# Kernel optimization log

Hardware: AMD Instinct MI355X
Metric: run time of the kernel (lower is better)

Reference implementation:

```python
import jax, jax.numpy as jnp
import numpy as np
import math

EPS = 1e-8
H, DM, S = 16, 1024, 128  # heads, d_model, seq_len (== channels)
DK = DM // H


def _fq_act_uint8(x):
    # Brevitas Uint8ActPerTensorFloat: per-tensor unsigned 8-bit fake-quant (negatives clip to 0)
    s = jnp.maximum(jnp.max(x), EPS) / 255.0
    return jnp.clip(jnp.round(x / s), 0.0, 255.0) * s


def _fq_w_int8(w):
    # Int8 weight per-tensor, narrow range [-127, 127]
    s = jnp.maximum(jnp.max(jnp.abs(w)), EPS) / 127.0
    return jnp.clip(jnp.round(w / s), -127.0, 127.0) * s, s


def _fq_pc_int8(x, axis):
    # QuantIdentity: signed 8-bit fake-quant, per-channel scale along `axis` (abs-max stats)
    red = tuple(i for i in range(x.ndim) if i != axis)
    s = jnp.maximum(jnp.max(jnp.abs(x), axis=red, keepdims=True), EPS) / 127.0
    return jnp.clip(jnp.round(x / s), -128.0, 127.0) * s


def _quant_linear(x, W, b):
    # QuantLinear: uint8 input quant, int8 weight quant, Int32 bias quant (scale = s_in * s_w)
    s_in = jnp.maximum(jnp.max(x), EPS) / 255.0
    xq = jnp.clip(jnp.round(x / s_in), 0.0, 255.0) * s_in
    Wq, s_w = _fq_w_int8(W)
    s_b = s_in * s_w
    bq = jnp.round(b / s_b) * s_b
    return jnp.einsum('bsd,od->bso', xq, Wq) + bq


def setup_inputs() -> dict:
    key = jax.random.key(0)
    ks = jax.random.split(key, 12)
    B = 64
    std = 1.0 / math.sqrt(DM)
    inp = {
        'query': jax.random.normal(ks[0], (B, S, DM), jnp.float32),
        'key':   jax.random.normal(ks[1], (B, S, DM), jnp.float32),
        'value': jax.random.normal(ks[2], (B, S, DM), jnp.float32),
        'mask':  jnp.ones((B, S, S), jnp.int32),
    }
    for i, nm in enumerate(['q', 'k', 'v', 'o']):
        inp[f'W{nm}'] = jax.random.normal(ks[3 + i], (DM, DM), jnp.float32) * std
        inp[f'b{nm}'] = jax.random.normal(ks[7 + i], (DM,), jnp.float32) * 0.01
    return inp


def reference(query, key, value, mask, Wq, bq, Wk, bk, Wv, bv, Wo, bo):
    B = query.shape[0]
    # QuantLinear projections -> [B, h, S, d_k]
    def proj(x, W, b):
        return _quant_linear(x, W, b).reshape(B, S, H, DK).transpose(0, 2, 1, 3)
    q = proj(query, Wq, bq)
    k = proj(key, Wk, bk)
    v = proj(value, Wv, bv)

    # quantizer_1: per-channel on q rows (axis 2); quantizer_2: on k^T columns (axis 3)
    kt = jnp.swapaxes(k, -2, -1)  # [B, h, d_k, S]
    scores = jnp.matmul(_fq_pc_int8(q, 2), _fq_pc_int8(kt, 3)) / math.sqrt(DK)
    scores = jnp.where(mask[:, None, :, :] == 0, -1e9, scores)
    p_attn = jax.nn.softmax(scores, axis=-1)

    # quantizer_3: per-channel on p_attn columns (axis 3); quantizer_4: on v rows (axis 2)
    x = jnp.matmul(_fq_pc_int8(p_attn, 3), _fq_pc_int8(v, 2))  # [B, h, S, d_k]
    x = x.transpose(0, 2, 1, 3).reshape(B, S, DM)
    return _quant_linear(x, Wo, bo)
```

## Files before the change

kernel.cpp:

```cpp
#include <hip/hip_runtime.h>
#include <hip/hip_bf16.h>
#include <math.h>

typedef unsigned short u16;
typedef unsigned int u32;
typedef unsigned long long u64;
typedef signed char i8;

constexpr int NB = 64, NS = 128, NDM = 1024, NH = 16, NDK = 64;
constexpr int NM = NB * NS;
constexpr float QEPS = 1e-8f;

typedef __attribute__((ext_vector_type(8))) short short8;
typedef __attribute__((ext_vector_type(4))) float f32x4;
typedef __attribute__((ext_vector_type(4))) int i32x4;

__device__ __forceinline__ u32 fenc(float f) {
  u32 u = __float_as_uint(f);
  return (u & 0x80000000u) ? ~u : (u | 0x80000000u);
}
__device__ __forceinline__ float fdec(u32 u) {
  u = (u & 0x80000000u) ? (u & 0x7FFFFFFFu) : ~u;
  return __uint_as_float(u);
}
__device__ __forceinline__ u16 f2bf(float f) { return (u16)(__float_as_uint(f) >> 16); }
__device__ __forceinline__ float bf2f(u16 u) { return __uint_as_float(((u32)u) << 16); }

__device__ __forceinline__ void glds16(const void* g, void* l) {
  __builtin_amdgcn_global_load_lds(
      (const __attribute__((address_space(1))) void*)(unsigned long long)(uintptr_t)g,
      (__attribute__((address_space(3))) void*)(u32)(uintptr_t)l, 16, 0, 0);
}


__global__ void maskbits_kernel(const int* __restrict__ mask, u64* __restrict__ mb,
                                u32* __restrict__ scl) {
  if (blockIdx.x == 0) {
    for (int i = threadIdx.x; i < 2048; i += blockDim.x) scl[i] = 0u;
  }
  int row = blockIdx.x * 4 + (threadIdx.x >> 6);
  int lane = threadIdx.x & 63;
  const int* mrow = mask + (size_t)row * NS;
  u64 b0 = __ballot(mrow[lane] != 0);
  u64 b1 = __ballot(mrow[64 + lane] != 0);
  if (lane == 0) { mb[row * 2] = b0; mb[row * 2 + 1] = b1; }
}

__global__ void fused_max_kernel(const float* __restrict__ q, const float* __restrict__ k,
                                 const float* __restrict__ v, const float* __restrict__ w0,
                                 const float* __restrict__ w1, const float* __restrict__ w2,
                                 const float* __restrict__ w3, u32* __restrict__ sclu) {
  int y = blockIdx.y;
  const float* src; size_t n4; int ab;
  switch (y) {
    case 0: src = q; n4 = (size_t)NM * NDM / 4; ab = 0; break;
    case 1: src = k; n4 = (size_t)NM * NDM / 4; ab = 0; break;
    case 2: src = v; n4 = (size_t)NM * NDM / 4; ab = 0; break;
    case 3: src = w0; n4 = (size_t)NDM * NDM / 4; ab = 1; break;
    case 4: src = w1; n4 = (size_t)NDM * NDM / 4; ab = 1; break;
    case 5: src = w2; n4 = (size_t)NDM * NDM / 4; ab = 1; break;
    default: src = w3; n4 = (size_t)NDM * NDM / 4; ab = 1; break;
  }
  float m = -INFINITY;
  size_t stride = (size_t)gridDim.x * blockDim.x;
  for (size_t i = (size_t)blockIdx.x * blockDim.x + threadIdx.x; i < n4; i += stride) {
    float4 f = ((const float4*)src)[i];
    if (ab) { f.x = fabsf(f.x); f.y = fabsf(f.y); f.z = fabsf(f.z); f.w = fabsf(f.w); }
    m = fmaxf(m, fmaxf(fmaxf(f.x, f.y), fmaxf(f.z, f.w)));
  }
  for (int off = 32; off; off >>= 1) m = fmaxf(m, __shfl_down(m, off));
  __shared__ float sm[4];
  if ((threadIdx.x & 63) == 0) sm[threadIdx.x >> 6] = m;
  __syncthreads();
  if (threadIdx.x == 0) {
    float r = fmaxf(fmaxf(sm[0], sm[1]), fmaxf(sm[2], sm[3]));
    atomicMax(&sclu[y], fenc(r));
  }
}

__global__ __launch_bounds__(256)
void quant_w_i8_kernel(const float* __restrict__ w0, const float* __restrict__ w1,
                       const float* __restrict__ w2, const float* __restrict__ w3,
                       i8* __restrict__ dst, int* __restrict__ colsum,
                       const u32* __restrict__ sclu) {
  int y = blockIdx.y, row = blockIdx.x, tid = threadIdx.x;
  const float* src = (y == 0 ? w0 : y == 1 ? w1 : y == 2 ? w2 : w3) + (size_t)row * NDM;
  float s = fmaxf(fdec(sclu[3 + y]), QEPS) / 127.0f;
  float4 f = ((const float4*)src)[tid];
  int a = (int)fminf(fmaxf(rintf(f.x / s), -127.f), 127.f);
  int b = (int)fminf(fmaxf(rintf(f.y / s), -127.f), 127.f);
  int c = (int)fminf(fmaxf(rintf(f.z / s), -127.f), 127.f);
  int d = (int)fminf(fmaxf(rintf(f.w / s), -127.f), 127.f);
  ((int*)(dst + (size_t)y * NDM * NDM + (size_t)row * NDM))[tid] =
      (a & 255) | ((b & 255) << 8) | ((c & 255) << 16) | ((d & 255) << 24);
  int ssum = a + b + c + d;
  for (int off = 32; off; off >>= 1) ssum += __shfl_down(ssum, off);
  __shared__ int sm[4];
  if ((tid & 63) == 0) sm[tid >> 6] = ssum;
  __syncthreads();
  if (tid == 0) colsum[y * NDM + row] = sm[0] + sm[1] + sm[2] + sm[3];
}

__global__ void quant_a_kernel(const float* __restrict__ s0, const float* __restrict__ s1,
                               const float* __restrict__ s2, i8* __restrict__ dst,
                               const u32* __restrict__ sclu, int slot_base) {
  int y = blockIdx.y;
  const float* src = y == 0 ? s0 : y == 1 ? s1 : s2;
  i8* d = dst + (size_t)y * NM * NDM;
  float s = fmaxf(fdec(sclu[slot_base + y]), QEPS) / 255.0f;
  size_t n4 = (size_t)NM * NDM / 4;
  size_t stride = (size_t)gridDim.x * blockDim.x;
  for (size_t i = (size_t)blockIdx.x * blockDim.x + threadIdx.x; i < n4; i += stride) {
    float4 f = ((const float4*)src)[i];
    int a = (int)fminf(fmaxf(rintf(f.x / s), 0.f), 255.f) - 128;
    int b = (int)fminf(fmaxf(rintf(f.y / s), 0.f), 255.f) - 128;
    int c = (int)fminf(fmaxf(rintf(f.z / s), 0.f), 255.f) - 128;
    int e = (int)fminf(fmaxf(rintf(f.w / s), 0.f), 255.f) - 128;
    ((int*)d)[i] = (a & 255) | ((b & 255) << 8) | ((c & 255) << 16) | ((e & 255) << 24);
  }
}

__global__ void qkv_i8_kernel(const float* __restrict__ projbase, i8* __restrict__ dstbase,
                              const float* __restrict__ scl) {
  int y = blockIdx.y;
  const float* src = projbase + (size_t)y * NM * NDM;
  i8* dst = dstbase + (size_t)y * NM * NDM;
  const float* sb = scl + 8 + y * 128;
  size_t n4 = (size_t)NM * NDM / 4;
  size_t stride = (size_t)gridDim.x * blockDim.x;
  for (size_t i = (size_t)blockIdx.x * blockDim.x + threadIdx.x; i < n4; i += stride) {
    int s_idx = (int)((i >> 8) & 127);
    float s = fmaxf(sb[s_idx], QEPS) / 127.0f;
    float4 f = ((const float4*)src)[i];
    int a = (int)fminf(fmaxf(rintf(f.x / s), -128.f), 127.f);
    int b = (int)fminf(fmaxf(rintf(f.y / s), -128.f), 127.f);
    int c = (int)fminf(fmaxf(rintf(f.z / s), -128.f), 127.f);
    int d = (int)fminf(fmaxf(rintf(f.w / s), -128.f), 127.f);
    ((int*)dst)[i] = (a & 255) | ((b & 255) << 8) | ((c & 255) << 16) | ((d & 255) << 24);
  }
}

constexpr int BM = 128, BN = 128, BK = 64;

template <bool PROJ>
__global__ __launch_bounds__(256)
void gemm_kernel(const i8* __restrict__ Abase, const i8* __restrict__ Wbase,
                 const int* __restrict__ colsum, const float* __restrict__ b0,
                 const float* __restrict__ b1, const float* __restrict__ b2,
                 float* __restrict__ Cbase, u32* __restrict__ sclu) {
  constexpr int K = NDM, N = NDM;
  const int z = PROJ ? blockIdx.z : 0;
  const i8* A = Abase + (size_t)z * NM * NDM;
  const i8* Wt = PROJ ? (Wbase + (size_t)z * NDM * NDM) : Wbase;
  const float* bias = PROJ ? (z == 0 ? b0 : z == 1 ? b1 : b2) : b0;
  float* C = PROJ ? (Cbase + (size_t)z * NM * NDM) : Cbase;
  const u32* slot_in = PROJ ? (sclu + z) : (sclu + 7);
  const u32* slot_w = PROJ ? (sclu + 3 + z) : (sclu + 6);
  const int* cs = colsum + (PROJ ? z : 3) * NDM;

  __shared__ __align__(16) i8 As[BM][BK];
  __shared__ __align__(16) i8 Bs[BN][BK];
  __shared__ float rmax2[2][BM];

  const int tid = threadIdx.x;
  const int lane = tid & 63, wave = tid >> 6;
  const int wm = (wave & 1) * 64, wn = (wave >> 1) * 64;
  const int r16 = lane & 15, quad = lane >> 4;
  const int bm = blockIdx.x * BM, bn = blockIdx.y * BN;

  i32x4 acc[4][4] = {};

  const int lrow = lane >> 2, lcol = (lane & 3) * 16;
  for (int k0 = 0; k0 < K; k0 += BK) {
    __syncthreads();
#pragma unroll
    for (int p = 0; p < 2; p++) {
      int r = wave * 32 + p * 16;
      glds16(A + (size_t)(bm + r + lrow) * K + k0 + lcol, &As[r][0]);
      glds16(Wt + (size_t)(bn + r + lrow) * K + k0 + lcol, &Bs[r][0]);
    }
    __syncthreads();
    i32x4 af[4], bfr[4];
#pragma unroll
    for (int i = 0; i < 4; i++) af[i] = *(const i32x4*)(&As[wm + i * 16 + r16][quad * 16]);
#pragma unroll
    for (int j = 0; j < 4; j++) bfr[j] = *(const i32x4*)(&Bs[wn + j * 16 + r16][quad * 16]);
#pragma unroll
    for (int i = 0; i < 4; i++)
#pragma unroll
      for (int j = 0; j < 4; j++)
        acc[i][j] = __builtin_amdgcn_mfma_i32_16x16x64_i8(af[i], bfr[j], acc[i][j], 0, 0, 0);
  }

  float s_in = fmaxf(fdec(*slot_in), QEPS) / 255.0f;
  float s_w = fmaxf(fdec(*slot_w), QEPS) / 127.0f;
  float sc = s_in * s_w;

  float bq[4];
  int csj[4];
#pragma unroll
  for (int j = 0; j < 4; j++) {
    int gc = bn + wn + j * 16 + r16;
    bq[j] = rintf(bias[gc] / sc) * sc;
    csj[j] = cs[gc] << 7;
  }
#pragma unroll
  for (int i = 0; i < 4; i++) {
#pragma unroll
    for (int r = 0; r < 4; r++) {
      int lr = wm + i * 16 + quad * 4 + r;
      int gr = bm + lr;
      float rm = 0.0f;
#pragma unroll
      for (int j = 0; j < 4; j++) {
        int gc = bn + wn + j * 16 + r16;
        float val = (float)(acc[i][j][r] + csj[j]) * sc + bq[j];
        C[(size_t)gr * N + gc] = val;
        if (PROJ) rm = fmaxf(rm, fabsf(val));
      }
      if (PROJ) {
#pragma unroll
        for (int off = 1; off < 16; off <<= 1) rm = fmaxf(rm, __shfl_xor(rm, off));
        if (r16 == 0) rmax2[wave >> 1][lr] = rm;
      }
    }
  }
  if (PROJ) {
    __syncthreads();
    if (tid < BM) {
      float m = fmaxf(rmax2[0][tid], rmax2[1][tid]);
      atomicMax((int*)&sclu[8 + z * 128 + tid], __float_as_int(m));
    }
  }
}

__global__ __launch_bounds__(256)
void attn_colmax_kernel(const i8* __restrict__ qi8, const i8* __restrict__ ki8,
                        const u64* __restrict__ mb, const float* __restrict__ scl,
                        float* __restrict__ cm_part) {
  const int bh = blockIdx.x, b = bh >> 4, h = bh & 15;
  const int tid = threadIdx.x, lane = tid & 63, wave = tid >> 6;
  const int r16 = lane & 15, quad = lane >> 4;

  __shared__ __align__(16) i8 Qs[NS][80];
  __shared__ __align__(16) i8 Ks[NS][80];
  __shared__ float sqv[NS], skv[NS];
  __shared__ float cmw[4][NS];

  {
    int row = tid >> 1, half = (tid & 1) * 32;
    const i8* qp = qi8 + (size_t)(b * NS + row) * NDM + h * NDK + half;
    const i8* kp = ki8 + (size_t)(b * NS + row) * NDM + h * NDK + half;
    *(int4*)&Qs[row][half] = *(const int4*)qp;
    *(int4*)&Qs[row][half + 16] = *(const int4*)(qp + 16);
    *(int4*)&Ks[row][half] = *(const int4*)kp;
    *(int4*)&Ks[row][half + 16] = *(const int4*)(kp + 16);
    if (tid < NS) {
      sqv[tid] = fmaxf(scl[8 + tid], QEPS) / 127.0f;
      skv[tid] = fmaxf(scl[8 + 128 + tid], QEPS) / 127.0f;
    }
  }
  __syncthreads();

  const int rowbase = wave * 32;
  i32x4 acc[2][8] = {};
#pragma unroll
  for (int mt = 0; mt < 2; mt++) {
    i32x4 a = *(const i32x4*)&Qs[rowbase + mt * 16 + r16][quad * 16];
#pragma unroll
    for (int nt = 0; nt < 8; nt++) {
      i32x4 bfrag = *(const i32x4*)&Ks[nt * 16 + r16][quad * 16];
      acc[mt][nt] = __builtin_amdgcn_mfma_i32_16x16x64_i8(a, bfrag, acc[mt][nt], 0, 0, 0);
    }
  }

  float skc[8], cm[8];
#pragma unroll
  for (int nt = 0; nt < 8; nt++) { skc[nt] = skv[nt * 16 + r16]; cm[nt] = 0.0f; }

#pragma unroll
  for (int mt = 0; mt < 2; mt++) {
#pragma unroll
    for (int r = 0; r < 4; r++) {
      int row = rowbase + mt * 16 + quad * 4 + r;
      float sq = sqv[row];
      const u64* mrow = mb + ((size_t)b * NS + row) * 2;
      u64 m0 = mrow[0], m1 = mrow[1];
      float vals[8];
      float mx = -INFINITY;
#pragma unroll
      for (int nt = 0; nt < 8; nt++) {
        float v = (float)acc[mt][nt][r] * (sq * skc[nt]) * 0.125f;
        u64 bits = nt < 4 ? m0 : m1;
        if (((bits >> ((nt * 16 + r16) & 63)) & 1ull) == 0) v = -1e9f;
        vals[nt] = v;
        mx = fmaxf(mx, v);
      }
#pragma unroll
      for (int off = 1; off < 16; off <<= 1) mx = fmaxf(mx, __shfl_xor(mx, off));
      float sum = 0.0f;
#pragma unroll
      for (int nt = 0; nt < 8; nt++) { vals[nt] = __expf(vals[nt] - mx); sum += vals[nt]; }
#pragma unroll
      for (int off = 1; off < 16; off <<= 1) sum += __shfl_xor(sum, off);
#pragma unroll
      for (int nt = 0; nt < 8; nt++) {
        float p = vals[nt] / sum;
        cm[nt] = fmaxf(cm[nt], p);
      }
    }
  }

#pragma unroll
  for (int nt = 0; nt < 8; nt++) {
    float c = cm[nt];
    c = fmaxf(c, __shfl_xor(c, 16));
    c = fmaxf(c, __shfl_xor(c, 32));
    if (quad == 0) cmw[wave][nt * 16 + r16] = c;
  }
  __syncthreads();
  if (tid < NS) {
    float c = fmaxf(fmaxf(cmw[0][tid], cmw[1][tid]), fmaxf(cmw[2][tid], cmw[3][tid]));
    cm_part[(size_t)tid * (NB * NH) + bh] = c;
  }
}

__global__ void colmax_reduce_kernel(const float* __restrict__ cm_part,
                                     u32* __restrict__ sclu) {
  int j = blockIdx.x;
  const float* row = cm_part + (size_t)j * (NB * NH);
  float m = 0.0f;
  for (int i = threadIdx.x; i < NB * NH; i += blockDim.x) m = fmaxf(m, row[i]);
  for (int off = 32; off; off >>= 1) m = fmaxf(m, __shfl_down(m, off));
  __shared__ float sm[4];
  if ((threadIdx.x & 63) == 0) sm[threadIdx.x >> 6] = m;
  __syncthreads();
  if (threadIdx.x == 0)
    sclu[392 + j] = __float_as_uint(fmaxf(fmaxf(sm[0], sm[1]), fmaxf(sm[2], sm[3])));
}

__global__ __launch_bounds__(256, 4)
void attn_pv2_kernel(const i8* __restrict__ qi8, const i8* __restrict__ ki8,
                     const i8* __restrict__ vi8, const u64* __restrict__ mb,
                     const float* __restrict__ scl, float* __restrict__ xout,
                     u32* __restrict__ xmax_slot) {
  const int bh = blockIdx.x, b = bh >> 4, h = bh & 15;
  const int tid = threadIdx.x, lane = tid & 63, wave = tid >> 6;
  const int r16 = lane & 15, quad = lane >> 4;
  const int rowbase = wave * 32;

  union SU {
    i8 K[NS][64];
    struct { u16 hi[64][72]; u16 lo[64][72]; } v;
  };
  __shared__ __align__(16) SU u;
  __shared__ __align__(16) u16 Ps[NS][72];
  __shared__ float sqv[NS], skv[NS], spv[NS], svv[NS];
  __shared__ float xmw[4];

  const int jl = tid >> 2, d0v = (tid & 3) * 16;
  const i8* vb = vi8 + (size_t)(b * NS + jl) * NDM + h * NDK + d0v;
  int4 vpre0 = *(const int4*)vb;
  int4 vpre1 = *(const int4*)(vb + (size_t)64 * NDM);

  i32x4 aq[2];
  {
    const i8* qp = qi8 + (size_t)b * NS * NDM + h * NDK;
#pragma unroll
    for (int mt = 0; mt < 2; mt++)
      aq[mt] = *(const i32x4*)(qp + (size_t)(rowbase + mt * 16 + r16) * NDM + quad * 16);
    const int lrow = lane >> 2, lcol = (lane & 3) * 16;
#pragma unroll
    for (int p = 0; p < 2; p++) {
      int r = wave * 32 + p * 16;
      glds16(ki8 + (size_t)(b * NS + r + lrow) * NDM + h * NDK + lcol, &u.K[r][0]);
    }
    if (tid < NS) {
      sqv[tid] = fmaxf(scl[8 + tid], QEPS) / 127.0f;
      skv[tid] = fmaxf(scl[8 + 128 + tid], QEPS) / 127.0f;
      spv[tid] = fmaxf(scl[392 + tid], QEPS) / 127.0f;
      svv[tid] = fmaxf(scl[8 + 256 + tid], QEPS) / 127.0f;
    }
  }
  __syncthreads();

  i32x4 acc[2][8] = {};
  __builtin_amdgcn_s_setprio(1);
#pragma unroll
  for (int mt = 0; mt < 2; mt++) {
#pragma unroll
    for (int nt = 0; nt < 8; nt++) {
      i32x4 bfrag = *(const i32x4*)&u.K[nt * 16 + r16][quad * 16];
      acc[mt][nt] = __builtin_amdgcn_mfma_i32_16x16x64_i8(aq[mt], bfrag, acc[mt][nt], 0, 0, 0);
    }
  }
  __builtin_amdgcn_s_setprio(0);

  float skc[8], spc[8];
#pragma unroll
  for (int nt = 0; nt < 8; nt++) {
    skc[nt] = skv[nt * 16 + r16];
    spc[nt] = spv[nt * 16 + r16];
  }

  u32 pqh[2][4][2];
#pragma unroll
  for (int mt = 0; mt < 2; mt++) {
#pragma unroll
    for (int r = 0; r < 4; r++) {
      int row = rowbase + mt * 16 + quad * 4 + r;
      float sq = sqv[row];
      const u64* mrow = mb + ((size_t)b * NS + row) * 2;
      u64 m0 = mrow[0], m1 = mrow[1];
      float vals[8];
      float mx = -INFINITY;
#pragma unroll
      for (int nt = 0; nt < 8; nt++) {
        float v = (float)acc[mt][nt][r] * (sq * skc[nt]) * 0.125f;
        u64 bits = nt < 4 ? m0 : m1;
        if (((bits >> ((nt * 16 + r16) & 63)) & 1ull) == 0) v = -1e9f;
        vals[nt] = v;
        mx = fmaxf(mx, v);
      }
#pragma unroll
      for (int off = 1; off < 16; off <<= 1) mx = fmaxf(mx, __shfl_xor(mx, off));
      float sum = 0.0f;
#pragma unroll
      for (int nt = 0; nt < 8; nt++) { vals[nt] = __expf(vals[nt] - mx); sum += vals[nt]; }
#pragma unroll
      for (int off = 1; off < 16; off <<= 1) sum += __shfl_xor(sum, off);
#pragma unroll
      for (int nt = 0; nt < 4; nt++) {
        float p = vals[nt] / sum;
        float pq = fminf(fmaxf(rintf(p / spc[nt]), -128.f), 127.f);
        Ps[row][nt * 16 + r16] = f2bf(pq);
      }
#pragma unroll
      for (int n2 = 0; n2 < 2; n2++) {
        float pa_ = vals[4 + n2 * 2] / sum;
        float pb_ = vals[5 + n2 * 2] / sum;
        float qa = fminf(fmaxf(rintf(pa_ / spc[4 + n2 * 2]), -128.f), 127.f);
        float qb = fminf(fmaxf(rintf(pb_ / spc[5 + n2 * 2]), -128.f), 127.f);
        pqh[mt][r][n2] = (u32)f2bf(qa) | ((u32)f2bf(qb) << 16);
      }
    }
  }

  f32x4 xacc[2][4] = {};
#pragma unroll
  for (int half = 0; half < 2; half++) {
    __syncthreads();
    {
      int j = half * 64 + jl;
      float g = spv[j] * svv[j];
      int4 raw = half ? vpre1 : vpre0;
      const i8* rb = (const i8*)&raw;
#pragma unroll
      for (int d = 0; d < 16; d++) {
        float w = (float)rb[d] * g;
        u16 hi = f2bf(w);
        u.v.hi[d0v + d][jl] = hi;
        u.v.lo[d0v + d][jl] = f2bf(w - bf2f(hi));
      }
    }
    __syncthreads();
    __builtin_amdgcn_s_setprio(1);
#pragma unroll
    for (int kk = 0; kk < 2; kk++) {
      short8 pa[2];
#pragma unroll
      for (int mt = 0; mt < 2; mt++)
        pa[mt] = *(const short8*)&Ps[rowbase + mt * 16 + r16][kk * 32 + quad * 8];
#pragma unroll
      for (int nt = 0; nt < 4; nt++) {
        short8 vh = *(const short8*)&u.v.hi[nt * 16 + r16][kk * 32 + quad * 8];
        short8 vl = *(const short8*)&u.v.lo[nt * 16 + r16][kk * 32 + quad * 8];
#pragma unroll
        for (int mt = 0; mt < 2; mt++) {
          xacc[mt][nt] = __builtin_amdgcn_mfma_f32_16x16x32_bf16(pa[mt], vh, xacc[mt][nt], 0, 0, 0);
          xacc[mt][nt] = __builtin_amdgcn_mfma_f32_16x16x32_bf16(pa[mt], vl, xacc[mt][nt], 0, 0, 0);
        }
      }
    }
    __builtin_amdgcn_s_setprio(0);
    if (half == 0) {
#pragma unroll
      for (int mt = 0; mt < 2; mt++)
#pragma unroll
        for (int r = 0; r < 4; r++) {
          int row = rowbase + mt * 16 + quad * 4 + r;
#pragma unroll
          for (int n2 = 0; n2 < 2; n2++) {
            u32 pk = pqh[mt][r][n2];
            Ps[row][(n2 * 2) * 16 + r16] = (u16)(pk & 0xFFFFu);
            Ps[row][(n2 * 2 + 1) * 16 + r16] = (u16)(pk >> 16);
          }
        }
    }
  }

  float mx = -INFINITY;
#pragma unroll
  for (int mt = 0; mt < 2; mt++)
#pragma unroll
    for (int nt = 0; nt < 4; nt++)
#pragma unroll
      for (int r = 0; r < 4; r++) {
        int row = rowbase + mt * 16 + quad * 4 + r;
        xout[((size_t)b * NS + row) * NDM + h * NDK + nt * 16 + r16] = xacc[mt][nt][r];
        mx = fmaxf(mx, xacc[mt][nt][r]);
      }
#pragma unroll
  for (int off = 1; off < 64; off <<= 1) mx = fmaxf(mx, __shfl_xor(mx, off));
  if (lane == 0) xmw[wave] = mx;
  __syncthreads();
  if (tid == 0) {
    float m = fmaxf(fmaxf(xmw[0], xmw[1]), fmaxf(xmw[2], xmw[3]));
    atomicMax(xmax_slot, fenc(m));
  }
}

constexpr size_t OFF_SCL = 0;
constexpr size_t OFF_CS  = 8192;
constexpr size_t OFF_MB  = OFF_CS + 4 * NDM * 4;
constexpr size_t OFF_W   = OFF_MB + (size_t)NM * 16;
constexpr size_t OFF_XQ  = OFF_W + 4 * (size_t)NDM * NDM;
constexpr size_t OFF_PQ  = OFF_XQ + 3 * (size_t)NM * NDM;
constexpr size_t OFF_I8  = OFF_PQ + 3 * (size_t)NM * NDM * 4;
constexpr size_t OFF_CM  = OFF_I8 + 3 * (size_t)NM * NDM;

extern "C" void kernel_launch(void* const* d_in, const int* in_sizes, int n_in,
                              void* d_out, int out_size, void* d_ws, size_t ws_size,
                              hipStream_t stream) {
  const float* query = (const float*)d_in[0];
  const float* key = (const float*)d_in[1];
  const float* value = (const float*)d_in[2];
  const int* mask = (const int*)d_in[3];
  const float* Wq = (const float*)d_in[4]; const float* bq = (const float*)d_in[5];
  const float* Wk = (const float*)d_in[6]; const float* bk = (const float*)d_in[7];
  const float* Wv = (const float*)d_in[8]; const float* bv = (const float*)d_in[9];
  const float* Wo = (const float*)d_in[10]; const float* bo = (const float*)d_in[11];

  char* ws = (char*)d_ws;
  float* scl = (float*)(ws + OFF_SCL);
  u32* sclu = (u32*)scl;
  int* colsum = (int*)(ws + OFF_CS);
  u64* mb = (u64*)(ws + OFF_MB);
  i8* wb = (i8*)(ws + OFF_W);
  i8* wob = wb + 3 * (size_t)NDM * NDM;
  i8* xq = (i8*)(ws + OFF_XQ);
  float* proj = (float*)(ws + OFF_PQ);
  i8* qkv8 = (i8*)(ws + OFF_I8);
  float* cm_part = (float*)(ws + OFF_CM);
  float* xout = proj + 2 * (size_t)NM * NDM;
  i8* vi8 = qkv8 + 2 * (size_t)NM * NDM;

  maskbits_kernel<<<NM / 4, 256, 0, stream>>>(mask, mb, sclu);
  fused_max_kernel<<<dim3(512, 7), 256, 0, stream>>>(query, key, value, Wq, Wk, Wv, Wo, sclu);
  quant_w_i8_kernel<<<dim3(NDM, 4), 256, 0, stream>>>(Wq, Wk, Wv, Wo, wb, colsum, sclu);
  quant_a_kernel<<<dim3(512, 3), 256, 0, stream>>>(query, key, value, xq, sclu, 0);

  gemm_kernel<true><<<dim3(NM / BM, NDM / BN, 3), 256, 0, stream>>>(
      xq, wb, colsum, bq, bk, bv, proj, sclu);

  qkv_i8_kernel<<<dim3(512, 3), 256, 0, stream>>>(proj, qkv8, scl);

  attn_colmax_kernel<<<NB * NH, 256, 0, stream>>>(qkv8, qkv8 + (size_t)NM * NDM, mb, scl,
                                                  cm_part);
  colmax_reduce_kernel<<<NS, 256, 0, stream>>>(cm_part, sclu);
  attn_pv2_kernel<<<NB * NH, 256, 0, stream>>>(qkv8, qkv8 + (size_t)NM * NDM, vi8, mb, scl,
                                               xout, sclu + 7);

  quant_a_kernel<<<dim3(512, 1), 256, 0, stream>>>(xout, xout, xout, xq, sclu, 7);
  gemm_kernel<false><<<dim3(NM / BM, NDM / BN, 1), 256, 0, stream>>>(
      xq, wob, colsum, bo, bo, bo, (float*)d_out, sclu);
}
```

Measured before the change: 388.5 us.

## Double-buffer int8 GEMM tiles, halve N tile, replace row-max atomics with reduction

The int8 projection GEMM now double-buffers its A/B shared-memory tiles so the next K-tile's global-to-LDS load overlaps the current MFMA work. It also shrinks the N tile to 64 and requests 4 blocks per CU via launch bounds. The per-row abs-max is no longer applied with global atomicMax; each block writes partial maxima to a workspace buffer and a new reduction kernel combines them. This trades one extra kernel launch and more blocks with lower per-block data reuse for better latency hiding and no atomic contention.

```diff
diff --git a/kernel.cpp b/kernel.cpp
--- a/kernel.cpp
+++ b/kernel.cpp
@@ -140,14 +140,15 @@
   }
 }
 
-constexpr int BM = 128, BN = 128, BK = 64;
+constexpr int BM = 128, BN = 64, BK = 64, KTILES = NDM / BK;
 
 template <bool PROJ>
-__global__ __launch_bounds__(256)
+__global__ __launch_bounds__(256, 4)
 void gemm_kernel(const i8* __restrict__ Abase, const i8* __restrict__ Wbase,
                  const int* __restrict__ colsum, const float* __restrict__ b0,
                  const float* __restrict__ b1, const float* __restrict__ b2,
-                 float* __restrict__ Cbase, u32* __restrict__ sclu) {
+                 float* __restrict__ Cbase, u32* __restrict__ sclu,
+                 float* __restrict__ rmax_part) {
   constexpr int K = NDM, N = NDM;
   const int z = PROJ ? blockIdx.z : 0;
   const i8* A = Abase + (size_t)z * NM * NDM;
@@ -158,48 +159,59 @@
   const u32* slot_w = PROJ ? (sclu + 3 + z) : (sclu + 6);
   const int* cs = colsum + (PROJ ? z : 3) * NDM;
 
-  __shared__ __align__(16) i8 As[BM][BK];
-  __shared__ __align__(16) i8 Bs[BN][BK];
-  __shared__ float rmax2[2][BM];
+  __shared__ __align__(16) i8 As[2][BM][BK];
+  __shared__ __align__(16) i8 Bs[2][BN][BK];
+  __shared__ float rmax2[4][64];
 
   const int tid = threadIdx.x;
   const int lane = tid & 63, wave = tid >> 6;
-  const int wm = (wave & 1) * 64, wn = (wave >> 1) * 64;
+  const int wm = (wave & 1) * 64, wn = (wave >> 1) * 32;
   const int r16 = lane & 15, quad = lane >> 4;
   const int bm = blockIdx.x * BM, bn = blockIdx.y * BN;
 
-  i32x4 acc[4][4] = {};
-
   const int lrow = lane >> 2, lcol = (lane & 3) * 16;
-  for (int k0 = 0; k0 < K; k0 += BK) {
+  const i8* Ab = A + (size_t)(bm + wave * 32 + lrow) * K + lcol;
+  const i8* Bb = Wt + (size_t)(bn + wave * 16 + lrow) * K + lcol;
+
+  i32x4 acc[4][2] = {};
+
+  glds16(Ab, &As[0][wave * 32][0]);
+  glds16(Ab + (size_t)16 * K, &As[0][wave * 32 + 16][0]);
+  glds16(Bb, &Bs[0][wave * 16][0]);
+  __syncthreads();
+
+  int cur = 0;
+  for (int t = 0; t < KTILES; t++) {
+    if (t + 1 < KTILES) {
+      int k0 = (t + 1) * BK;
+      glds16(Ab + k0, &As[cur ^ 1][wave * 32][0]);
+      glds16(Ab + (size_t)16 * K + k0, &As[cur ^ 1][wave * 32 + 16][0]);
+      glds16(Bb + k0, &Bs[cur ^ 1][wave * 16][0]);
+    }
+    i32x4 af[4], bfr[2];
+#pragma unroll
+    for (int i = 0; i < 4; i++)
+      af[i] = *(const i32x4*)(&As[cur][wm + i * 16 + r16][quad * 16]);
+#pragma unroll
+    for (int j = 0; j < 2; j++)
+      bfr[j] = *(const i32x4*)(&Bs[cur][wn + j * 16 + r16][quad * 16]);
+#pragma unroll
+    for (int i = 0; i < 4; i++)
+#pragma unroll
+      for (int j = 0; j < 2; j++)
+        acc[i][j] = __builtin_amdgcn_mfma_i32_16x16x64_i8(af[i], bfr[j], acc[i][j], 0, 0, 0);
     __syncthreads();
-#pragma unroll
-    for (int p = 0; p < 2; p++) {
-      int r = wave * 32 + p * 16;
-      glds16(A + (size_t)(bm + r + lrow) * K + k0 + lcol, &As[r][0]);
-      glds16(Wt + (size_t)(bn + r + lrow) * K + k0 + lcol, &Bs[r][0]);
-    }
-    __syncthreads();
-    i32x4 af[4], bfr[4];
-#pragma unroll
-    for (int i = 0; i < 4; i++) af[i] = *(const i32x4*)(&As[wm + i * 16 + r16][quad * 16]);
-#pragma unroll
-    for (int j = 0; j < 4; j++) bfr[j] = *(const i32x4*)(&Bs[wn + j * 16 + r16][quad * 16]);
-#pragma unroll
-    for (int i = 0; i < 4; i++)
-#pragma unroll
-      for (int j = 0; j < 4; j++)
-        acc[i][j] = __builtin_amdgcn_mfma_i32_16x16x64_i8(af[i], bfr[j], acc[i][j], 0, 0, 0);
+    cur ^= 1;
   }
 
   float s_in = fmaxf(fdec(*slot_in), QEPS) / 255.0f;
   float s_w = fmaxf(fdec(*slot_w), QEPS) / 127.0f;
   float sc = s_in * s_w;
 
-  float bq[4];
-  int csj[4];
-#pragma unroll
-  for (int j = 0; j < 4; j++) {
+  float bq[2];
+  int csj[2];
+#pragma unroll
+  for (int j = 0; j < 2; j++) {
     int gc = bn + wn + j * 16 + r16;
     bq[j] = rintf(bias[gc] / sc) * sc;
     csj[j] = cs[gc] << 7;
@@ -208,11 +220,11 @@
   for (int i = 0; i < 4; i++) {
 #pragma unroll
     for (int r = 0; r < 4; r++) {
-      int lr = wm + i * 16 + quad * 4 + r;
-      int gr = bm + lr;
+      int l64 = i * 16 + quad * 4 + r;
+      int gr = bm + wm + l64;
       float rm = 0.0f;
 #pragma unroll
-      for (int j = 0; j < 4; j++) {
+      for (int j = 0; j < 2; j++) {
         int gc = bn + wn + j * 16 + r16;
         float val = (float)(acc[i][j][r] + csj[j]) * sc + bq[j];
         C[(size_t)gr * N + gc] = val;
@@ -221,17 +233,33 @@
       if (PROJ) {
 #pragma unroll
         for (int off = 1; off < 16; off <<= 1) rm = fmaxf(rm, __shfl_xor(rm, off));
-        if (r16 == 0) rmax2[wave >> 1][lr] = rm;
+        if (r16 == 0) rmax2[wave][l64] = rm;
       }
     }
   }
   if (PROJ) {
     __syncthreads();
     if (tid < BM) {
-      float m = fmaxf(rmax2[0][tid], rmax2[1][tid]);
-      atomicMax((int*)&sclu[8 + z * 128 + tid], __float_as_int(m));
-    }
-  }
+      int g = tid >> 6, l = tid & 63;
+      float m = fmaxf(rmax2[g][l], rmax2[g + 2][l]);
+      int blockId = z * 1024 + blockIdx.x * 16 + blockIdx.y;
+      rmax_part[(size_t)blockId * 128 + tid] = m;
+    }
+  }
+}
+
+__global__ void rmax_reduce_kernel(const float* __restrict__ part, u32* __restrict__ sclu) {
+  int slot = blockIdx.x;
+  int z = slot >> 7, lr = slot & 127;
+  const float* base = part + (size_t)z * 1024 * 128 + lr;
+  float m = 0.0f;
+  for (int i = threadIdx.x; i < 1024; i += blockDim.x) m = fmaxf(m, base[(size_t)i * 128]);
+  for (int off = 32; off; off >>= 1) m = fmaxf(m, __shfl_down(m, off));
+  __shared__ float sm[4];
+  if ((threadIdx.x & 63) == 0) sm[threadIdx.x >> 6] = m;
+  __syncthreads();
+  if (threadIdx.x == 0)
+    sclu[8 + slot] = __float_as_uint(fmaxf(fmaxf(sm[0], sm[1]), fmaxf(sm[2], sm[3])));
 }
 
 __global__ __launch_bounds__(256)
@@ -528,6 +556,7 @@
 constexpr size_t OFF_PQ  = OFF_XQ + 3 * (size_t)NM * NDM;
 constexpr size_t OFF_I8  = OFF_PQ + 3 * (size_t)NM * NDM * 4;
 constexpr size_t OFF_CM  = OFF_I8 + 3 * (size_t)NM * NDM;
+constexpr size_t OFF_RP  = OFF_CM + (size_t)NS * NB * NH * 4;
 
 extern "C" void kernel_launch(void* const* d_in, const int* in_sizes, int n_in,
                               void* d_out, int out_size, void* d_ws, size_t ws_size,
@@ -552,6 +581,7 @@
   float* proj = (float*)(ws + OFF_PQ);
   i8* qkv8 = (i8*)(ws + OFF_I8);
   float* cm_part = (float*)(ws + OFF_CM);
+  float* rmax_part = (float*)(ws + OFF_RP);
   float* xout = proj + 2 * (size_t)NM * NDM;
   i8* vi8 = qkv8 + 2 * (size_t)NM * NDM;
 
@@ -561,7 +591,8 @@
   quant_a_kernel<<<dim3(512, 3), 256, 0, stream>>>(query, key, value, xq, sclu, 0);
 
   gemm_kernel<true><<<dim3(NM / BM, NDM / BN, 3), 256, 0, stream>>>(
-      xq, wb, colsum, bq, bk, bv, proj, sclu);
+      xq, wb, colsum, bq, bk, bv, proj, sclu, rmax_part);
+  rmax_reduce_kernel<<<384, 256, 0, stream>>>(rmax_part, sclu);
 
   qkv_i8_kernel<<<dim3(512, 3), 256, 0, stream>>>(proj, qkv8, scl);
 
@@ -573,5 +604,5 @@
 
   quant_a_kernel<<<dim3(512, 1), 256, 0, stream>>>(xout, xout, xout, xq, sclu, 7);
   gemm_kernel<false><<<dim3(NM / BM, NDM / BN, 1), 256, 0, stream>>>(
-      xq, wob, colsum, bo, bo, bo, (float*)d_out, sclu);
-}
+      xq, wob, colsum, bo, bo, bo, (float*)d_out, sclu, rmax_part);
+}
```

After: 390.9 us. About the same (+0.6%).
